# Optimization experiments

Measured on AMD Instinct MI355X. Metric: run time of the kernel, lower is better.

## Reference

```python
import jax, jax.numpy as jnp
import numpy as np

B, S, D = 8, 4096, 1024


def setup_inputs() -> dict:
    key = jax.random.key(0)
    k = jax.random.split(key, 6)
    scale = 1.0 / np.sqrt(D)  # torch nn.Linear default init range
    x = jax.random.normal(k[0], (B, S, D), dtype=jnp.float32)
    mask = jnp.ones((B, S), dtype=jnp.float32)
    Wu = jax.random.uniform(k[1], (D, D), jnp.float32, -scale, scale)
    bu = jax.random.uniform(k[2], (D,), jnp.float32, -scale, scale)
    Wf = jax.random.uniform(k[3], (D, D), jnp.float32, -scale, scale)
    bf = jax.random.uniform(k[4], (D,), jnp.float32, -scale, scale)
    decay_param = jnp.zeros((1,), dtype=jnp.float32)
    return {"x": x, "mask": mask, "Wu": Wu, "bu": bu, "Wf": Wf, "bf": bf, "decay_param": decay_param}


def reference(x, mask, Wu, bu, Wf, bf, decay_param):
    # decay is a learned scalar in (0,1)
    decay = jax.nn.sigmoid(decay_param)[0]
    # Batch linear_update over all timesteps at once: (B,S,D)
    upd = jnp.einsum('bsd,ed->bse', x, Wu) + bu
    m = mask[..., None]  # (B,S,1)
    # mask-gated recurrence: mem_t = a_t * mem_{t-1} + b_t
    #   a_t = mask*decay + (1-mask),  b_t = mask*update
    a = m * decay + (1.0 - m)
    b = m * upd
    a_s = jnp.swapaxes(a, 0, 1)  # (S,B,1)
    b_s = jnp.swapaxes(b, 0, 1)  # (S,B,D)

    def step(mem, ab):
        a_t, b_t = ab
        mem = a_t * mem + b_t
        return mem, mem

    mem0 = jnp.zeros((B, D), dtype=x.dtype)
    _, mem_seq = jax.lax.scan(step, mem0, (a_s, b_s))  # (S,B,D)
    mem_seq = jnp.swapaxes(mem_seq, 0, 1)  # (B,S,D)
    # Batch linear_f over all timesteps
    out = jnp.einsum('bsd,ed->bse', mem_seq, Wf) + bf
    return out
```

## Files before the change

kernel.cpp:

```cpp
#include <hip/hip_runtime.h>
#include <hip/hip_bf16.h>
#include <math.h>

#define PB 8
#define PS 4096
#define PD 1024

typedef __attribute__((ext_vector_type(8))) short bf16x8;
typedef __attribute__((ext_vector_type(4))) float f32x4;

__device__ __forceinline__ ushort f2b(float f) {
    unsigned u = __float_as_uint(f);
    unsigned r = (u + 0x7FFFu + ((u >> 16) & 1u)) >> 16;
    return (ushort)r;
}
__device__ __forceinline__ float b2f(ushort h) {
    return __uint_as_float(((unsigned)h) << 16);
}

__device__ __forceinline__ void gl2lds16(const void* g, void* l) {
    __builtin_amdgcn_global_load_lds(
        (const __attribute__((address_space(1))) void*)g,
        (__attribute__((address_space(3))) void*)l, 16, 0, 0);
}

__global__ __launch_bounds__(256) void cvt_f32_bf16(const float* __restrict__ in,
                                                    ushort* __restrict__ out, int n) {
    int i = (blockIdx.x * 256 + threadIdx.x) * 4;
    if (i + 3 < n) {
        float4 v = *(const float4*)(in + i);
        ushort4 o;
        o.x = f2b(v.x); o.y = f2b(v.y); o.z = f2b(v.z); o.w = f2b(v.w);
        *(ushort4*)(out + i) = o;
    }
}

__global__ __launch_bounds__(256) void cvt_w2(const float* __restrict__ Wu,
                                              const float* __restrict__ Wf,
                                              ushort* __restrict__ Wub,
                                              ushort* __restrict__ Wfb, int n) {
    int i = (blockIdx.x * 256 + threadIdx.x) * 4;
    const float* in = (i < n) ? Wu : Wf;
    ushort* out = (i < n) ? Wub : Wfb;
    int j = (i < n) ? i : i - n;
    float4 v = *(const float4*)(in + j);
    ushort4 o;
    o.x = f2b(v.x); o.y = f2b(v.y); o.z = f2b(v.z); o.w = f2b(v.w);
    *(ushort4*)(out + j) = o;
}

template <bool OUT_BF16>
__global__ __launch_bounds__(256) void gemm_bt(const ushort* __restrict__ A,
                                               const ushort* __restrict__ Bm,
                                               const float* __restrict__ bias,
                                               void* __restrict__ C,
                                               int M, int N, int K) {
    __shared__ ushort As[128 * 64];
    __shared__ ushort Bs[128 * 64];

    const int tid = threadIdx.x;
    const int lane = tid & 63;
    const int wave = tid >> 6;
    const int nbn = N >> 7;
    const int xcd = blockIdx.x & 7;
    const int g = blockIdx.x >> 3;
    const int bm = xcd * ((M >> 7) >> 3) + g / nbn;
    const int bn = g % nbn;
    const int wm = wave >> 1, wn = wave & 1;
    const int l15 = lane & 15, quad = lane >> 4;

    const int srow = wave * 8 + (lane >> 3);
    const int sgx = ((lane & 7) ^ ((lane >> 3) & 7)) * 8;
    const ushort* Ag = A + (size_t)(bm * 128 + srow) * K + sgx;
    const ushort* Bg = Bm + (size_t)(bn * 128 + srow) * K + sgx;
    ushort* Asw = As + wave * 8 * 64;
    ushort* Bsw = Bs + wave * 8 * 64;

    f32x4 acc[4][4];
#pragma unroll
    for (int i = 0; i < 4; ++i)
#pragma unroll
        for (int j = 0; j < 4; ++j) acc[i][j] = (f32x4){0.f, 0.f, 0.f, 0.f};

    const int rsw = l15 & 7;

    for (int k0 = 0; k0 < K; k0 += 64) {
        __syncthreads();
#pragma unroll
        for (int b = 0; b < 4; ++b) {
            gl2lds16(Ag + k0 + (size_t)(b * 32) * K, Asw + b * 32 * 64);
            gl2lds16(Bg + k0 + (size_t)(b * 32) * K, Bsw + b * 32 * 64);
        }
        __syncthreads();

#pragma unroll
        for (int p = 0; p < 2; ++p) {
            const int aoff = ((p * 4 + quad) ^ rsw) * 8;
            bf16x8 af[4], bfr[4];
#pragma unroll
            for (int i = 0; i < 4; ++i)
                af[i] = *(const bf16x8*)(As + (wm * 64 + i * 16 + l15) * 64 + aoff);
#pragma unroll
            for (int j = 0; j < 4; ++j)
                bfr[j] = *(const bf16x8*)(Bs + (wn * 64 + j * 16 + l15) * 64 + aoff);
#pragma unroll
            for (int i = 0; i < 4; ++i)
#pragma unroll
                for (int j = 0; j < 4; ++j)
                    acc[i][j] = __builtin_amdgcn_mfma_f32_16x16x32_bf16(af[i], bfr[j], acc[i][j], 0, 0, 0);
        }
    }

    const int gm0 = bm * 128 + wm * 64;
    const int gn0 = bn * 128 + wn * 64;
    float bv[4];
#pragma unroll
    for (int j = 0; j < 4; ++j) bv[j] = bias[gn0 + j * 16 + l15];
#pragma unroll
    for (int i = 0; i < 4; ++i) {
#pragma unroll
        for (int j = 0; j < 4; ++j) {
            const int col = gn0 + j * 16 + l15;
#pragma unroll
            for (int r = 0; r < 4; ++r) {
                const int row = gm0 + i * 16 + quad * 4 + r;
                float v = acc[i][j][r] + bv[j];
                if (OUT_BF16)
                    ((ushort*)C)[(size_t)row * N + col] = f2b(v);
                else
                    ((float*)C)[(size_t)row * N + col] = v;
            }
        }
    }
}

__global__ __launch_bounds__(256) void scan_partial(const ushort* __restrict__ upd,
                                                    const float* __restrict__ mask,
                                                    const float* __restrict__ dp,
                                                    float* __restrict__ Bc,
                                                    float* __restrict__ Ac,
                                                    int S, int D, int C) {
    const int c = blockIdx.x % C;
    const int b = blockIdx.x / C;
    const int L = S / C;
    const int d0 = threadIdx.x * 4;
    const float decay = 1.f / (1.f + expf(-dp[0]));
    const ushort* up = upd + ((size_t)b * S + (size_t)c * L) * D + d0;
    const float* mp = mask + (size_t)b * S + (size_t)c * L;
    float aA = 1.f;
    float b0 = 0.f, b1 = 0.f, b2 = 0.f, b3 = 0.f;
    for (int s0 = 0; s0 < L; s0 += 4) {
        float4 mv = *(const float4*)(mp + s0);
        ushort4 u0 = *(const ushort4*)(up + (size_t)(s0 + 0) * D);
        ushort4 u1 = *(const ushort4*)(up + (size_t)(s0 + 1) * D);
        ushort4 u2 = *(const ushort4*)(up + (size_t)(s0 + 2) * D);
        ushort4 u3 = *(const ushort4*)(up + (size_t)(s0 + 3) * D);
        float m, a;
        m = mv.x; a = m * decay + (1.f - m); aA *= a;
        b0 = a * b0 + m * b2f(u0.x); b1 = a * b1 + m * b2f(u0.y);
        b2 = a * b2 + m * b2f(u0.z); b3 = a * b3 + m * b2f(u0.w);
        m = mv.y; a = m * decay + (1.f - m); aA *= a;
        b0 = a * b0 + m * b2f(u1.x); b1 = a * b1 + m * b2f(u1.y);
        b2 = a * b2 + m * b2f(u1.z); b3 = a * b3 + m * b2f(u1.w);
        m = mv.z; a = m * decay + (1.f - m); aA *= a;
        b0 = a * b0 + m * b2f(u2.x); b1 = a * b1 + m * b2f(u2.y);
        b2 = a * b2 + m * b2f(u2.z); b3 = a * b3 + m * b2f(u2.w);
        m = mv.w; a = m * decay + (1.f - m); aA *= a;
        b0 = a * b0 + m * b2f(u3.x); b1 = a * b1 + m * b2f(u3.y);
        b2 = a * b2 + m * b2f(u3.z); b3 = a * b3 + m * b2f(u3.w);
    }
    *(float4*)(Bc + (size_t)blockIdx.x * D + d0) = make_float4(b0, b1, b2, b3);
    if (threadIdx.x == 0) Ac[blockIdx.x] = aA;
}

__global__ __launch_bounds__(256) void scan_prefix(const float* __restrict__ Ac,
                                                   const float* __restrict__ Bc,
                                                   float* __restrict__ Mn, int D, int C) {
    int gid = blockIdx.x * 256 + threadIdx.x;
    int b = gid / D;
    int d = gid - b * D;
    float mem = 0.f;
    for (int c = 0; c < C; c += 4) {
        float4 av = *(const float4*)(Ac + b * C + c);
        size_t i0 = ((size_t)(b * C + c)) * D + d;
        float q0 = Bc[i0];
        float q1 = Bc[i0 + D];
        float q2 = Bc[i0 + 2 * (size_t)D];
        float q3 = Bc[i0 + 3 * (size_t)D];
        Mn[i0] = mem;                    mem = av.x * mem + q0;
        Mn[i0 + D] = mem;                mem = av.y * mem + q1;
        Mn[i0 + 2 * (size_t)D] = mem;    mem = av.z * mem + q2;
        Mn[i0 + 3 * (size_t)D] = mem;    mem = av.w * mem + q3;
    }
}

__global__ __launch_bounds__(256) void scan_final(const ushort* __restrict__ upd,
                                                  const float* __restrict__ mask,
                                                  const float* __restrict__ dp,
                                                  const float* __restrict__ Mn,
                                                  ushort* __restrict__ ms,
                                                  int S, int D, int C) {
    const int c = blockIdx.x % C;
    const int b = blockIdx.x / C;
    const int L = S / C;
    const int d0 = threadIdx.x * 4;
    const float decay = 1.f / (1.f + expf(-dp[0]));
    const ushort* up = upd + ((size_t)b * S + (size_t)c * L) * D + d0;
    ushort* op = ms + ((size_t)b * S + (size_t)c * L) * D + d0;
    const float* mp = mask + (size_t)b * S + (size_t)c * L;
    float4 m0 = *(const float4*)(Mn + (size_t)blockIdx.x * D + d0);
    float v0 = m0.x, v1 = m0.y, v2 = m0.z, v3 = m0.w;
    for (int s0 = 0; s0 < L; s0 += 4) {
        float4 mv = *(const float4*)(mp + s0);
        ushort4 u0 = *(const ushort4*)(up + (size_t)(s0 + 0) * D);
        ushort4 u1 = *(const ushort4*)(up + (size_t)(s0 + 1) * D);
        ushort4 u2 = *(const ushort4*)(up + (size_t)(s0 + 2) * D);
        ushort4 u3 = *(const ushort4*)(up + (size_t)(s0 + 3) * D);
        float m, a;
        ushort4 o;
        m = mv.x; a = m * decay + (1.f - m);
        v0 = a * v0 + m * b2f(u0.x); v1 = a * v1 + m * b2f(u0.y);
        v2 = a * v2 + m * b2f(u0.z); v3 = a * v3 + m * b2f(u0.w);
        o.x = f2b(v0); o.y = f2b(v1); o.z = f2b(v2); o.w = f2b(v3);
        *(ushort4*)(op + (size_t)(s0 + 0) * D) = o;
        m = mv.y; a = m * decay + (1.f - m);
        v0 = a * v0 + m * b2f(u1.x); v1 = a * v1 + m * b2f(u1.y);
        v2 = a * v2 + m * b2f(u1.z); v3 = a * v3 + m * b2f(u1.w);
        o.x = f2b(v0); o.y = f2b(v1); o.z = f2b(v2); o.w = f2b(v3);
        *(ushort4*)(op + (size_t)(s0 + 1) * D) = o;
        m = mv.z; a = m * decay + (1.f - m);
        v0 = a * v0 + m * b2f(u2.x); v1 = a * v1 + m * b2f(u2.y);
        v2 = a * v2 + m * b2f(u2.z); v3 = a * v3 + m * b2f(u2.w);
        o.x = f2b(v0); o.y = f2b(v1); o.z = f2b(v2); o.w = f2b(v3);
        *(ushort4*)(op + (size_t)(s0 + 2) * D) = o;
        m = mv.w; a = m * decay + (1.f - m);
        v0 = a * v0 + m * b2f(u3.x); v1 = a * v1 + m * b2f(u3.y);
        v2 = a * v2 + m * b2f(u3.z); v3 = a * v3 + m * b2f(u3.w);
        o.x = f2b(v0); o.y = f2b(v1); o.z = f2b(v2); o.w = f2b(v3);
        *(ushort4*)(op + (size_t)(s0 + 3) * D) = o;
    }
}

extern "C" void kernel_launch(void* const* d_in, const int* in_sizes, int n_in,
                              void* d_out, int out_size, void* d_ws, size_t ws_size,
                              hipStream_t stream) {
    const float* x    = (const float*)d_in[0];
    const float* mask = (const float*)d_in[1];
    const float* Wu   = (const float*)d_in[2];
    const float* bu   = (const float*)d_in[3];
    const float* Wf   = (const float*)d_in[4];
    const float* bfv  = (const float*)d_in[5];
    const float* dp   = (const float*)d_in[6];

    const int B = PB, S = PS, D = PD;
    const int M = B * S;
    const int C = 128;

    char* ws = (char*)d_ws;
    ushort* xb   = (ushort*)(ws);
    ushort* updb = (ushort*)(ws + 67108864);
    ushort* memb = (ushort*)(ws + 134217728);
    ushort* Wub  = (ushort*)(ws + 201326592);
    ushort* Wfb  = (ushort*)(ws + 203423744);
    float*  Bc   = (float*)(ws + 205520896);
    float*  Mn   = (float*)(ws + 209715200);
    float*  Ac   = (float*)(ws + 213909504);

    const int nx = B * S * D;
    cvt_f32_bf16<<<nx / 1024, 256, 0, stream>>>(x, xb, nx);
    cvt_w2<<<(2 * D * D) / 1024, 256, 0, stream>>>(Wu, Wf, Wub, Wfb, D * D);

    dim3 g1((M / 128) * (D / 128));
    gemm_bt<true><<<g1, 256, 0, stream>>>(xb, Wub, bu, (void*)updb, M, D, D);

    scan_partial<<<B * C, 256, 0, stream>>>(updb, mask, dp, Bc, Ac, S, D, C);
    scan_prefix<<<(B * D) / 256, 256, 0, stream>>>(Ac, Bc, Mn, D, C);
    scan_final<<<B * C, 256, 0, stream>>>(updb, mask, dp, Mn, memb, S, D, C);

    gemm_bt<false><<<g1, 256, 0, stream>>>(memb, Wfb, bfv, d_out, M, D, D);
}
```

Baseline: 466.1 us.

## Enlarge GEMM tiles to 256x256 with 512 threads and double-buffered LDS

The bf16 GEMM moves from 128x128 tiles with 256 threads to 256x256 tiles with 8 waves, each wave computing a 128x64 sub-tile. LDS is double-buffered so global-to-LDS loads for tile t+2 overlap with MFMA on tile t, using explicit vmcnt waits and barriers. MFMA blocks are wrapped in s_setprio. The goal is better operand reuse per load and hiding memory latency, at the cost of 128 KB of LDS per block and higher register use, which limits occupancy.

```diff
diff --git a/kernel.cpp b/kernel.cpp
--- a/kernel.cpp
+++ b/kernel.cpp
@@ -50,74 +50,95 @@
 }
 
 template <bool OUT_BF16>
-__global__ __launch_bounds__(256) void gemm_bt(const ushort* __restrict__ A,
-                                               const ushort* __restrict__ Bm,
-                                               const float* __restrict__ bias,
-                                               void* __restrict__ C,
-                                               int M, int N, int K) {
-    __shared__ ushort As[128 * 64];
-    __shared__ ushort Bs[128 * 64];
+__global__ __launch_bounds__(512, 2) void gemm_bt(const ushort* __restrict__ A,
+                                                  const ushort* __restrict__ Bm,
+                                                  const float* __restrict__ bias,
+                                                  void* __restrict__ C,
+                                                  int M, int N, int K) {
+    __shared__ ushort As[2][256 * 64];
+    __shared__ ushort Bs[2][256 * 64];
 
     const int tid = threadIdx.x;
     const int lane = tid & 63;
     const int wave = tid >> 6;
-    const int nbn = N >> 7;
+    const int nbn = N >> 8;
     const int xcd = blockIdx.x & 7;
     const int g = blockIdx.x >> 3;
-    const int bm = xcd * ((M >> 7) >> 3) + g / nbn;
+    const int bpx = (gridDim.x >> 3) / nbn;
+    const int bm = xcd * bpx + g / nbn;
     const int bn = g % nbn;
-    const int wm = wave >> 1, wn = wave & 1;
+    const int wm = wave >> 2, wn = wave & 3;
     const int l15 = lane & 15, quad = lane >> 4;
 
     const int srow = wave * 8 + (lane >> 3);
     const int sgx = ((lane & 7) ^ ((lane >> 3) & 7)) * 8;
-    const ushort* Ag = A + (size_t)(bm * 128 + srow) * K + sgx;
-    const ushort* Bg = Bm + (size_t)(bn * 128 + srow) * K + sgx;
-    ushort* Asw = As + wave * 8 * 64;
-    ushort* Bsw = Bs + wave * 8 * 64;
-
-    f32x4 acc[4][4];
-#pragma unroll
-    for (int i = 0; i < 4; ++i)
+    const ushort* Ag = A + (size_t)(bm * 256 + srow) * K + sgx;
+    const ushort* Bg = Bm + (size_t)(bn * 256 + srow) * K + sgx;
+    const int lbase = wave * 8 * 64;
+
+#define STAGE_TILE(kk, cc)                                                      \
+    do {                                                                        \
+        _Pragma("unroll")                                                       \
+        for (int rb = 0; rb < 4; ++rb) {                                        \
+            gl2lds16(Ag + (kk) + (size_t)(rb * 64) * K, &As[cc][rb * 4096 + lbase]); \
+            gl2lds16(Bg + (kk) + (size_t)(rb * 64) * K, &Bs[cc][rb * 4096 + lbase]); \
+        }                                                                       \
+    } while (0)
+
+    f32x4 acc[8][4];
+#pragma unroll
+    for (int i = 0; i < 8; ++i)
 #pragma unroll
         for (int j = 0; j < 4; ++j) acc[i][j] = (f32x4){0.f, 0.f, 0.f, 0.f};
 
-    const int rsw = l15 & 7;
-
-    for (int k0 = 0; k0 < K; k0 += 64) {
-        __syncthreads();
-#pragma unroll
-        for (int b = 0; b < 4; ++b) {
-            gl2lds16(Ag + k0 + (size_t)(b * 32) * K, Asw + b * 32 * 64);
-            gl2lds16(Bg + k0 + (size_t)(b * 32) * K, Bsw + b * 32 * 64);
-        }
-        __syncthreads();
-
+    const int nt = K >> 6;
+
+    STAGE_TILE(0, 0);
+    STAGE_TILE(64, 1);
+    asm volatile("s_waitcnt vmcnt(8)" ::: "memory");
+    __builtin_amdgcn_s_barrier();
+
+    for (int t = 0; t < nt; ++t) {
+        const int c = t & 1;
+        const ushort* Ab = &As[c][(wm * 128 + l15) * 64];
+        const ushort* Bb = &Bs[c][(wn * 64 + l15) * 64];
 #pragma unroll
         for (int p = 0; p < 2; ++p) {
-            const int aoff = ((p * 4 + quad) ^ rsw) * 8;
-            bf16x8 af[4], bfr[4];
-#pragma unroll
-            for (int i = 0; i < 4; ++i)
-                af[i] = *(const bf16x8*)(As + (wm * 64 + i * 16 + l15) * 64 + aoff);
+            const int aoff = ((p * 4 + quad) ^ (l15 & 7)) * 8;
+            bf16x8 af[8], bfr[4];
+#pragma unroll
+            for (int i = 0; i < 8; ++i)
+                af[i] = *(const bf16x8*)(Ab + i * 16 * 64 + aoff);
 #pragma unroll
             for (int j = 0; j < 4; ++j)
-                bfr[j] = *(const bf16x8*)(Bs + (wn * 64 + j * 16 + l15) * 64 + aoff);
-#pragma unroll
-            for (int i = 0; i < 4; ++i)
+                bfr[j] = *(const bf16x8*)(Bb + j * 16 * 64 + aoff);
+            __builtin_amdgcn_s_setprio(1);
+#pragma unroll
+            for (int i = 0; i < 8; ++i)
 #pragma unroll
                 for (int j = 0; j < 4; ++j)
                     acc[i][j] = __builtin_amdgcn_mfma_f32_16x16x32_bf16(af[i], bfr[j], acc[i][j], 0, 0, 0);
+            __builtin_amdgcn_s_setprio(0);
         }
-    }
-
-    const int gm0 = bm * 128 + wm * 64;
-    const int gn0 = bn * 128 + wn * 64;
+        asm volatile("s_waitcnt lgkmcnt(0)" ::: "memory");
+        __builtin_amdgcn_s_barrier();
+        if (t + 2 < nt) {
+            STAGE_TILE((t + 2) * 64, c);
+            asm volatile("s_waitcnt vmcnt(8)" ::: "memory");
+        } else {
+            asm volatile("s_waitcnt vmcnt(0)" ::: "memory");
+        }
+        __builtin_amdgcn_s_barrier();
+    }
+#undef STAGE_TILE
+
+    const int gm0 = bm * 256 + wm * 128;
+    const int gn0 = bn * 256 + wn * 64;
     float bv[4];
 #pragma unroll
     for (int j = 0; j < 4; ++j) bv[j] = bias[gn0 + j * 16 + l15];
 #pragma unroll
-    for (int i = 0; i < 4; ++i) {
+    for (int i = 0; i < 8; ++i) {
 #pragma unroll
         for (int j = 0; j < 4; ++j) {
             const int col = gn0 + j * 16 + l15;
@@ -270,12 +291,12 @@
     cvt_f32_bf16<<<nx / 1024, 256, 0, stream>>>(x, xb, nx);
     cvt_w2<<<(2 * D * D) / 1024, 256, 0, stream>>>(Wu, Wf, Wub, Wfb, D * D);
 
-    dim3 g1((M / 128) * (D / 128));
-    gemm_bt<true><<<g1, 256, 0, stream>>>(xb, Wub, bu, (void*)updb, M, D, D);
+    dim3 g1((M / 256) * (D / 256));
+    gemm_bt<true><<<g1, 512, 0, stream>>>(xb, Wub, bu, (void*)updb, M, D, D);
 
     scan_partial<<<B * C, 256, 0, stream>>>(updb, mask, dp, Bc, Ac, S, D, C);
     scan_prefix<<<(B * D) / 256, 256, 0, stream>>>(Ac, Bc, Mn, D, C);
     scan_final<<<B * C, 256, 0, stream>>>(updb, mask, dp, Mn, memb, S, D, C);
 
-    gemm_bt<false><<<g1, 256, 0, stream>>>(memb, Wfb, bfv, d_out, M, D, D);
-}
+    gemm_bt<false><<<g1, 512, 0, stream>>>(memb, Wfb, bfv, d_out, M, D, D);
+}
```

Result: faster. 442.8 us (-5.0%).
